# Performance work log

Measured on AMD Instinct MI355X. Metric: run time of the kernel, lower is better.

## Reference

```python
import jax, jax.numpy as jnp
import numpy as np


def setup_inputs() -> dict:
    key = jax.random.key(0)
    k1, k2, k3 = jax.random.split(key, 3)
    B, C_in, H, W = 32, 128, 64, 64
    C_out, KH, KW = 256, 3, 3
    x = jax.random.normal(k1, (B, C_in, H, W), dtype=jnp.float32)
    # kaiming_normal fan_out scale ~ sqrt(2 / (C_out*KH*KW)); plain normal is fine for a numeric reference
    weight = jax.random.normal(k2, (C_out, C_in, KH, KW), dtype=jnp.float32) * (2.0 / (C_out * KH * KW)) ** 0.5
    fan_in = C_in * KH * KW
    bound = 1.0 / (fan_in ** 0.5)
    bias = jax.random.uniform(k3, (C_out,), dtype=jnp.float32, minval=-bound, maxval=bound)
    return {"x": x, "weight": weight, "bias": bias}


def reference(x, weight, bias):
    # Equivalent of unfold (im2col) + matmul + fold with stride=1, padding=1:
    # a standard 2D convolution in NCHW/OIHW layout.
    out = jax.lax.conv_general_dilated(
        x, weight,
        window_strides=(1, 1),
        padding=((1, 1), (1, 1)),
        dimension_numbers=("NCHW", "OIHW", "NCHW"),
    )
    return out + bias[None, :, None, None]
```

## Files before the change

### kernel.cpp

```cpp
#include <hip/hip_runtime.h>

typedef __attribute__((ext_vector_type(4))) int   v4i;
typedef __attribute__((ext_vector_type(8))) short s8;
typedef __attribute__((ext_vector_type(4))) float f32x4;
typedef __attribute__((ext_vector_type(16))) float f32x16;

#define GLB __attribute__((address_space(1)))
#define LDS_AS __attribute__((address_space(3)))

__device__ __forceinline__ unsigned short f2bf(float f) {
  unsigned u = __builtin_bit_cast(unsigned, f);
  return (unsigned short)((u + 0x7fffu + ((u >> 16) & 1u)) >> 16);
}

__global__ void prep(const float* __restrict__ x, const float* __restrict__ w,
                     unsigned int* __restrict__ xw, unsigned short* __restrict__ ww) {
  int t = threadIdx.x;
  if (blockIdx.x >= 2048) {
    int o = (blockIdx.x - 2048) * 256 + t;
    int tap = o >> 15;
    int c   = (o >> 13) & 3;
    int cog = (o >> 10) & 7;
    int kk  = (o >> 9) & 1;
    int lh  = (o >> 8) & 1;
    int l31 = (o >> 3) & 31;
    int e   = o & 7;
    int co = cog * 32 + l31;
    int ci = c * 32 + kk * 16 + lh * 8 + e;
    ww[o] = f2bf(w[(co * 128 + ci) * 9 + tap]);
    return;
  }
  __shared__ float tile[128][65];
  int bid = blockIdx.x;
  int b = bid >> 6, h = bid & 63;
  {
    int wcol4 = (t & 15) * 4, cl = t >> 4;
    const float* src = x + ((size_t)(b * 128) * 64 + h) * 64 + wcol4;
#pragma unroll
    for (int j = 0; j < 8; ++j) {
      int ci = j * 16 + cl;
      f32x4 v = *(const f32x4*)(src + (size_t)ci * 4096);
      tile[ci][wcol4 + 0] = v[0];
      tile[ci][wcol4 + 1] = v[1];
      tile[ci][wcol4 + 2] = v[2];
      tile[ci][wcol4 + 3] = v[3];
    }
  }
  unsigned int* dst = xw + (size_t)((b * 66 + h + 1) * 66) * 64;
  if (t < 128) {
    int col = (t >> 6) ? 65 : 0;
    dst[(size_t)col * 64 + (t & 63)] = 0u;
  }
  if (h == 0 || h == 63) {
    unsigned int* rb = xw + (size_t)(b * 66 + (h == 0 ? 0 : 65)) * 66 * 64;
    for (int j = t; j < 66 * 64; j += 256) rb[j] = 0u;
  }
  __syncthreads();
  {
    int ci2 = (t & 63) * 2, wl = t >> 6;
#pragma unroll
    for (int j = 0; j < 16; ++j) {
      int wcol = j * 4 + wl;
      unsigned p = (unsigned)f2bf(tile[ci2][wcol]) |
                   ((unsigned)f2bf(tile[ci2 + 1][wcol]) << 16);
      dst[(size_t)(wcol + 1) * 64 + (t & 63)] = p;
    }
  }
}

__global__ __launch_bounds__(256, 3) void conv_mfma(
    const unsigned short* __restrict__ xw, const unsigned short* __restrict__ ww,
    const float* __restrict__ bias, float* __restrict__ out) {
  __shared__ unsigned short Xl[204 * 128];
  const int tid = threadIdx.x;
  const int lane = tid & 63;
  const int l31 = lane & 31, lh = lane >> 5;
  const int mw = tid >> 6;
  int bid = blockIdx.x;
  bid = (bid & 7) * 256 + (bid >> 3);
  const int b = bid >> 6, h0 = bid & 63;
  const unsigned xlb = (unsigned)(unsigned long long)((LDS_AS void*)Xl);

  {
    const char* xbase = (const char*)xw;
#pragma unroll
    for (int it = 0; it < 13; ++it) {
      int s = tid + it * 256;
      if (s < 3264) {
        int q = s >> 4, p = s & 15;
        int u = p ^ (q & 15);
        int rr = q / 68, cc = q - rr * 68;
        if (cc > 65) cc = 65;
        unsigned src = (unsigned)((b * 66 + h0 + rr) * 66 + cc) * 256u + (unsigned)u * 16u;
        __builtin_amdgcn_global_load_lds((const GLB unsigned int*)(xbase + src),
                                         (LDS_AS unsigned int*)&Xl[s * 8], 16, 0, 0);
      }
    }
  }

  f32x16 acc[2][2];
#pragma unroll
  for (int m = 0; m < 2; ++m)
#pragma unroll
    for (int n = 0; n < 2; ++n)
#pragma unroll
      for (int e = 0; e < 16; ++e) acc[m][n][e] = 0.f;

  v4i areg[3][4];
  v4i breg[2][4];
  const unsigned abyte = (unsigned)(mw * 4096 + lane * 16);

  #define ALOAD_ASM(slot, step)                                               \
    do {                                                                      \
      unsigned _wo = (unsigned)(step) * 16384u + abyte;                       \
      asm volatile("global_load_dwordx4 %0, %1, %2 offset:0"                  \
                   : "=v"(areg[slot][0]) : "v"(_wo), "s"(ww));                \
      asm volatile("global_load_dwordx4 %0, %1, %2 offset:1024"               \
                   : "=v"(areg[slot][1]) : "v"(_wo), "s"(ww));                \
      asm volatile("global_load_dwordx4 %0, %1, %2 offset:2048"               \
                   : "=v"(areg[slot][2]) : "v"(_wo), "s"(ww));                \
      asm volatile("global_load_dwordx4 %0, %1, %2 offset:3072"               \
                   : "=v"(areg[slot][3]) : "v"(_wo), "s"(ww));                \
    } while (0)

  #define BLOAD_ASM(slot, S)                                                  \
    do {                                                                      \
      const int _t = (S) >> 2, _c = (S) & 3;                                  \
      const int _kh = _t / 3, _kw = _t - _kh * 3;                             \
      const int _q0 = _kh * 68 + _kw + l31;                                   \
      const int _xq = (_q0 & 15) ^ lh;             \
      unsigned _a0 = xlb + (unsigned)((_q0 << 8) + (((_c * 4) ^ _xq) << 4));  \
      unsigned _a1 = xlb + (unsigned)((_q0 << 8) + (((_c * 4 + 2) ^ _xq) << 4)); \
      asm volatile("ds_read_b128 %0, %1" : "=v"(breg[slot][0]) : "v"(_a0));   \
      asm volatile("ds_read_b128 %0, %1 offset:8192"                          \
                   : "=v"(breg[slot][1]) : "v"(_a0));                         \
      asm volatile("ds_read_b128 %0, %1" : "=v"(breg[slot][2]) : "v"(_a1));   \
      asm volatile("ds_read_b128 %0, %1 offset:8192"                          \
                   : "=v"(breg[slot][3]) : "v"(_a1));                         \
    } while (0)

  #define KSTEP(S)                                                            \
    do {                                                                      \
      const int _s = (S);                                                     \
      if (_s < 34) ALOAD_ASM((_s + 2) % 3, _s + 2);                           \
      if (_s < 35) BLOAD_ASM((_s + 1) & 1, _s + 1);                           \
      if (_s < 34)                                                            \
        asm volatile("s_waitcnt vmcnt(8) lgkmcnt(4)" ::: "memory");           \
      else if (_s == 34)                                                      \
        asm volatile("s_waitcnt vmcnt(4) lgkmcnt(4)" ::: "memory");           \
      else                                                                    \
        asm volatile("s_waitcnt vmcnt(0) lgkmcnt(0)" ::: "memory");           \
      __builtin_amdgcn_sched_barrier(0);                                      \
      const int _cs = _s % 3, _bs = _s & 1;                                   \
      __builtin_amdgcn_s_setprio(1);                                          \
      acc[0][0] = __builtin_amdgcn_mfma_f32_32x32x16_bf16(__builtin_bit_cast(s8, areg[_cs][0]), __builtin_bit_cast(s8, breg[_bs][0]), acc[0][0], 0, 0, 0); \
      acc[1][0] = __builtin_amdgcn_mfma_f32_32x32x16_bf16(__builtin_bit_cast(s8, areg[_cs][2]), __builtin_bit_cast(s8, breg[_bs][0]), acc[1][0], 0, 0, 0); \
      acc[0][1] = __builtin_amdgcn_mfma_f32_32x32x16_bf16(__builtin_bit_cast(s8, areg[_cs][0]), __builtin_bit_cast(s8, breg[_bs][1]), acc[0][1], 0, 0, 0); \
      acc[1][1] = __builtin_amdgcn_mfma_f32_32x32x16_bf16(__builtin_bit_cast(s8, areg[_cs][2]), __builtin_bit_cast(s8, breg[_bs][1]), acc[1][1], 0, 0, 0); \
      acc[0][0] = __builtin_amdgcn_mfma_f32_32x32x16_bf16(__builtin_bit_cast(s8, areg[_cs][1]), __builtin_bit_cast(s8, breg[_bs][2]), acc[0][0], 0, 0, 0); \
      acc[1][0] = __builtin_amdgcn_mfma_f32_32x32x16_bf16(__builtin_bit_cast(s8, areg[_cs][3]), __builtin_bit_cast(s8, breg[_bs][2]), acc[1][0], 0, 0, 0); \
      acc[0][1] = __builtin_amdgcn_mfma_f32_32x32x16_bf16(__builtin_bit_cast(s8, areg[_cs][1]), __builtin_bit_cast(s8, breg[_bs][3]), acc[0][1], 0, 0, 0); \
      acc[1][1] = __builtin_amdgcn_mfma_f32_32x32x16_bf16(__builtin_bit_cast(s8, areg[_cs][3]), __builtin_bit_cast(s8, breg[_bs][3]), acc[1][1], 0, 0, 0); \
      __builtin_amdgcn_s_setprio(0);                                          \
    } while (0)

  ALOAD_ASM(0, 0);
  ALOAD_ASM(1, 1);
  asm volatile("s_waitcnt vmcnt(8)" ::: "memory");
  __builtin_amdgcn_sched_barrier(0);
  __builtin_amdgcn_s_barrier();
  BLOAD_ASM(0, 0);

#pragma unroll
  for (int s = 0; s < 36; ++s) KSTEP(s);

#pragma unroll
  for (int m = 0; m < 2; ++m)
#pragma unroll
    for (int rq = 0; rq < 4; ++rq) {
      const int cob = mw * 64 + m * 32 + 8 * rq + 4 * lh;
      const f32x4 bi = *(const f32x4*)(bias + cob);
#pragma unroll
      for (int n = 0; n < 2; ++n) {
        const int wc = n * 32 + l31;
        size_t base = ((size_t)(b * 256 + cob) * 64 + h0) * 64 + wc;
#pragma unroll
        for (int e = 0; e < 4; ++e)
          out[base + (size_t)e * 4096] = acc[m][n][rq * 4 + e] + bi[e];
      }
    }
}

__global__ void conv_naive(const float* __restrict__ x, const float* __restrict__ w,
                           const float* __restrict__ bias, float* __restrict__ out) {
  int i = blockIdx.x * 256 + threadIdx.x;
  int wc = i & 63, h = (i >> 6) & 63, co = (i >> 12) & 255, b = i >> 20;
  float s = bias[co];
  for (int ci = 0; ci < 128; ++ci)
#pragma unroll
    for (int kh = 0; kh < 3; ++kh) {
      int hh = h + kh - 1;
      if ((unsigned)hh >= 64u) continue;
#pragma unroll
      for (int kw = 0; kw < 3; ++kw) {
        int wg = wc + kw - 1;
        if ((unsigned)wg >= 64u) continue;
        s += x[((b * 128 + ci) * 64 + hh) * 64 + wg] *
             w[((co * 128 + ci) * 3 + kh) * 3 + kw];
      }
    }
  out[i] = s;
}

extern "C" void kernel_launch(void* const* d_in, const int* in_sizes, int n_in,
                              void* d_out, int out_size, void* d_ws, size_t ws_size,
                              hipStream_t stream) {
  const float* x    = (const float*)d_in[0];
  const float* w    = (const float*)d_in[1];
  const float* bias = (const float*)d_in[2];
  float* out = (float*)d_out;

  const size_t X_OFF  = 1ull << 20;
  const size_t XBYTES = 32ull * 66 * 66 * 128 * 2;
  const size_t NEED   = X_OFF + XBYTES;

  if (ws_size >= NEED) {
    unsigned short* ww = (unsigned short*)d_ws;
    unsigned short* xq = (unsigned short*)((char*)d_ws + X_OFF);
    hipLaunchKernelGGL(prep, dim3(3200), dim3(256), 0, stream, x, w,
                       (unsigned int*)xq, ww);
    hipLaunchKernelGGL(conv_mfma, dim3(2048), dim3(256), 0, stream, xq, ww, bias, out);
  } else {
    hipLaunchKernelGGL(conv_naive, dim3(131072), dim3(256), 0, stream, x, w, bias, out);
  }
}
```

Before: 95.63 us.

## Split output channels across two blocks to double grid and occupancy

Each block now computes 128 output channels instead of 256 for one output row, which doubles the grid to 4096 blocks. It halves the accumulator and weight-register footprint per wave so launch bounds can rise to 4 blocks per SM. The wait counts are adjusted to match the reduced load count. The trade-off is that each input tile is staged into LDS twice, once per channel half, which doubles LDS fill traffic and the im2col loads, and each block's MFMA-to-load ratio drops.

```diff
diff --git a/kernel.cpp b/kernel.cpp
--- a/kernel.cpp
+++ b/kernel.cpp
@@ -68,7 +68,7 @@
   }
 }
 
-__global__ __launch_bounds__(256, 3) void conv_mfma(
+__global__ __launch_bounds__(256, 4) void conv_mfma(
     const unsigned short* __restrict__ xw, const unsigned short* __restrict__ ww,
     const float* __restrict__ bias, float* __restrict__ out) {
   __shared__ unsigned short Xl[204 * 128];
@@ -77,8 +77,10 @@
   const int l31 = lane & 31, lh = lane >> 5;
   const int mw = tid >> 6;
   int bid = blockIdx.x;
-  bid = (bid & 7) * 256 + (bid >> 3);
-  const int b = bid >> 6, h0 = bid & 63;
+  bid = (bid & 7) * 512 + (bid >> 3);
+  const int co_t = bid & 1;
+  const int pt = bid >> 1;
+  const int b = pt >> 6, h0 = pt & 63;
   const unsigned xlb = (unsigned)(unsigned long long)((LDS_AS void*)Xl);
 
   {
@@ -98,17 +100,15 @@
     }
   }
 
-  f32x16 acc[2][2];
-#pragma unroll
-  for (int m = 0; m < 2; ++m)
-#pragma unroll
-    for (int n = 0; n < 2; ++n)
-#pragma unroll
-      for (int e = 0; e < 16; ++e) acc[m][n][e] = 0.f;
-
-  v4i areg[3][4];
+  f32x16 acc[2];
+#pragma unroll
+  for (int n = 0; n < 2; ++n)
+#pragma unroll
+    for (int e = 0; e < 16; ++e) acc[n][e] = 0.f;
+
+  v4i areg[3][2];
   v4i breg[2][4];
-  const unsigned abyte = (unsigned)(mw * 4096 + lane * 16);
+  const unsigned abyte = (unsigned)(co_t * 8192 + mw * 2048 + lane * 16);
 
   #define ALOAD_ASM(slot, step)                                               \
     do {                                                                      \
@@ -117,10 +117,6 @@
                    : "=v"(areg[slot][0]) : "v"(_wo), "s"(ww));                \
       asm volatile("global_load_dwordx4 %0, %1, %2 offset:1024"               \
                    : "=v"(areg[slot][1]) : "v"(_wo), "s"(ww));                \
-      asm volatile("global_load_dwordx4 %0, %1, %2 offset:2048"               \
-                   : "=v"(areg[slot][2]) : "v"(_wo), "s"(ww));                \
-      asm volatile("global_load_dwordx4 %0, %1, %2 offset:3072"               \
-                   : "=v"(areg[slot][3]) : "v"(_wo), "s"(ww));                \
     } while (0)
 
   #define BLOAD_ASM(slot, S)                                                  \
@@ -145,28 +141,24 @@
       if (_s < 34) ALOAD_ASM((_s + 2) % 3, _s + 2);                           \
       if (_s < 35) BLOAD_ASM((_s + 1) & 1, _s + 1);                           \
       if (_s < 34)                                                            \
-        asm volatile("s_waitcnt vmcnt(8) lgkmcnt(4)" ::: "memory");           \
+        asm volatile("s_waitcnt vmcnt(4) lgkmcnt(4)" ::: "memory");           \
       else if (_s == 34)                                                      \
-        asm volatile("s_waitcnt vmcnt(4) lgkmcnt(4)" ::: "memory");           \
+        asm volatile("s_waitcnt vmcnt(2) lgkmcnt(4)" ::: "memory");           \
       else                                                                    \
         asm volatile("s_waitcnt vmcnt(0) lgkmcnt(0)" ::: "memory");           \
       __builtin_amdgcn_sched_barrier(0);                                      \
       const int _cs = _s % 3, _bs = _s & 1;                                   \
       __builtin_amdgcn_s_setprio(1);                                          \
-      acc[0][0] = __builtin_amdgcn_mfma_f32_32x32x16_bf16(__builtin_bit_cast(s8, areg[_cs][0]), __builtin_bit_cast(s8, breg[_bs][0]), acc[0][0], 0, 0, 0); \
-      acc[1][0] = __builtin_amdgcn_mfma_f32_32x32x16_bf16(__builtin_bit_cast(s8, areg[_cs][2]), __builtin_bit_cast(s8, breg[_bs][0]), acc[1][0], 0, 0, 0); \
-      acc[0][1] = __builtin_amdgcn_mfma_f32_32x32x16_bf16(__builtin_bit_cast(s8, areg[_cs][0]), __builtin_bit_cast(s8, breg[_bs][1]), acc[0][1], 0, 0, 0); \
-      acc[1][1] = __builtin_amdgcn_mfma_f32_32x32x16_bf16(__builtin_bit_cast(s8, areg[_cs][2]), __builtin_bit_cast(s8, breg[_bs][1]), acc[1][1], 0, 0, 0); \
-      acc[0][0] = __builtin_amdgcn_mfma_f32_32x32x16_bf16(__builtin_bit_cast(s8, areg[_cs][1]), __builtin_bit_cast(s8, breg[_bs][2]), acc[0][0], 0, 0, 0); \
-      acc[1][0] = __builtin_amdgcn_mfma_f32_32x32x16_bf16(__builtin_bit_cast(s8, areg[_cs][3]), __builtin_bit_cast(s8, breg[_bs][2]), acc[1][0], 0, 0, 0); \
-      acc[0][1] = __builtin_amdgcn_mfma_f32_32x32x16_bf16(__builtin_bit_cast(s8, areg[_cs][1]), __builtin_bit_cast(s8, breg[_bs][3]), acc[0][1], 0, 0, 0); \
-      acc[1][1] = __builtin_amdgcn_mfma_f32_32x32x16_bf16(__builtin_bit_cast(s8, areg[_cs][3]), __builtin_bit_cast(s8, breg[_bs][3]), acc[1][1], 0, 0, 0); \
+      acc[0] = __builtin_amdgcn_mfma_f32_32x32x16_bf16(__builtin_bit_cast(s8, areg[_cs][0]), __builtin_bit_cast(s8, breg[_bs][0]), acc[0], 0, 0, 0); \
+      acc[1] = __builtin_amdgcn_mfma_f32_32x32x16_bf16(__builtin_bit_cast(s8, areg[_cs][0]), __builtin_bit_cast(s8, breg[_bs][1]), acc[1], 0, 0, 0); \
+      acc[0] = __builtin_amdgcn_mfma_f32_32x32x16_bf16(__builtin_bit_cast(s8, areg[_cs][1]), __builtin_bit_cast(s8, breg[_bs][2]), acc[0], 0, 0, 0); \
+      acc[1] = __builtin_amdgcn_mfma_f32_32x32x16_bf16(__builtin_bit_cast(s8, areg[_cs][1]), __builtin_bit_cast(s8, breg[_bs][3]), acc[1], 0, 0, 0); \
       __builtin_amdgcn_s_setprio(0);                                          \
     } while (0)
 
   ALOAD_ASM(0, 0);
   ALOAD_ASM(1, 1);
-  asm volatile("s_waitcnt vmcnt(8)" ::: "memory");
+  asm volatile("s_waitcnt vmcnt(4)" ::: "memory");
   __builtin_amdgcn_sched_barrier(0);
   __builtin_amdgcn_s_barrier();
   BLOAD_ASM(0, 0);
@@ -175,20 +167,18 @@
   for (int s = 0; s < 36; ++s) KSTEP(s);
 
 #pragma unroll
-  for (int m = 0; m < 2; ++m)
-#pragma unroll
-    for (int rq = 0; rq < 4; ++rq) {
-      const int cob = mw * 64 + m * 32 + 8 * rq + 4 * lh;
-      const f32x4 bi = *(const f32x4*)(bias + cob);
-#pragma unroll
-      for (int n = 0; n < 2; ++n) {
-        const int wc = n * 32 + l31;
-        size_t base = ((size_t)(b * 256 + cob) * 64 + h0) * 64 + wc;
-#pragma unroll
-        for (int e = 0; e < 4; ++e)
-          out[base + (size_t)e * 4096] = acc[m][n][rq * 4 + e] + bi[e];
-      }
-    }
+  for (int rq = 0; rq < 4; ++rq) {
+    const int cob = co_t * 128 + mw * 32 + 8 * rq + 4 * lh;
+    const f32x4 bi = *(const f32x4*)(bias + cob);
+#pragma unroll
+    for (int n = 0; n < 2; ++n) {
+      const int wc = n * 32 + l31;
+      size_t base = ((size_t)(b * 256 + cob) * 64 + h0) * 64 + wc;
+#pragma unroll
+      for (int e = 0; e < 4; ++e)
+        out[base + (size_t)e * 4096] = acc[n][rq * 4 + e] + bi[e];
+    }
+  }
 }
 
 __global__ void conv_naive(const float* __restrict__ x, const float* __restrict__ w,
@@ -229,7 +219,7 @@
     unsigned short* xq = (unsigned short*)((char*)d_ws + X_OFF);
     hipLaunchKernelGGL(prep, dim3(3200), dim3(256), 0, stream, x, w,
                        (unsigned int*)xq, ww);
-    hipLaunchKernelGGL(conv_mfma, dim3(2048), dim3(256), 0, stream, xq, ww, bias, out);
+    hipLaunchKernelGGL(conv_mfma, dim3(4096), dim3(256), 0, stream, xq, ww, bias, out);
   } else {
     hipLaunchKernelGGL(conv_naive, dim3(131072), dim3(256), 0, stream, x, w, bias, out);
   }
```

Measured after the change: 98.49 us. 3.0% more time.
